# Kernel optimization log

Measured on AMD Instinct MI355X. Metric: run time of the kernel, lower is better.

The kernel has to match this reference:

```python
import jax, jax.numpy as jnp
import numpy as np

N_NODES = 65536
N_EDGES = 524288
N_LAYERS = 3
D = 128
ED = 32
BATCH = 64
NEG_SLOPE = 0.2


def setup_inputs() -> dict:
    key = jax.random.key(0)
    ks = jax.random.split(key, 10)
    w_scale = 1.0 / np.sqrt(D)
    return {
        "x": jax.random.normal(ks[0], (N_NODES, D), dtype=jnp.float32),
        "edge_index": jax.random.randint(ks[1], (2, N_EDGES), 0, N_NODES, dtype=jnp.int32),
        "edge_attr": jax.random.normal(ks[2], (N_EDGES, ED), dtype=jnp.float32),
        "Ws": jax.random.normal(ks[3], (N_LAYERS, D, D), dtype=jnp.float32) * w_scale,
        "att_src": jax.random.normal(ks[4], (N_LAYERS, D), dtype=jnp.float32) * w_scale,
        "att_dst": jax.random.normal(ks[5], (N_LAYERS, D), dtype=jnp.float32) * w_scale,
        "W_edge": jax.random.normal(ks[6], (N_LAYERS, ED, D), dtype=jnp.float32) * (1.0 / np.sqrt(ED)),
        "att_edge": jax.random.normal(ks[7], (N_LAYERS, D), dtype=jnp.float32) * w_scale,
        "bias": jnp.zeros((N_LAYERS, D), dtype=jnp.float32),
        "batch_size": BATCH,
    }


def _gat_layer(x, src, dst, ea, W, a_s, a_d, We, a_e, b, n):
    # PyG GATConv, heads=1, concat=True, flow source_to_target.
    h = x @ W                                      # [N, D]
    al = (h @ a_s)[src] + (h @ a_d)[dst] + (ea @ We) @ a_e   # [E]
    al = jax.nn.leaky_relu(al, NEG_SLOPE)
    # segment softmax over destination-node neighborhoods
    m = jax.ops.segment_max(al, dst, num_segments=n)
    ex = jnp.exp(al - m[dst])
    den = jax.ops.segment_sum(ex, dst, num_segments=n)
    w = ex / den[dst]                              # [E]
    out = jax.ops.segment_sum(w[:, None] * h[src], dst, num_segments=n)
    return out + b


def reference(x, edge_index, edge_attr, Ws, att_src, att_dst, W_edge, att_edge, bias, batch_size):
    n = x.shape[0]
    # add_self_loops with fill_value='mean': self-loop edge_attr is the mean of
    # incoming edge features per destination node (zero if no incoming edges).
    loop = jnp.arange(n, dtype=edge_index.dtype)
    src = jnp.concatenate([edge_index[0], loop])
    dst = jnp.concatenate([edge_index[1], loop])
    cnt = jax.ops.segment_sum(jnp.ones((edge_attr.shape[0],), edge_attr.dtype), edge_index[1], num_segments=n)
    fill = jax.ops.segment_sum(edge_attr, edge_index[1], num_segments=n) / jnp.maximum(cnt, 1.0)[:, None]
    ea = jnp.concatenate([edge_attr, fill], axis=0)

    h = x
    for l in range(Ws.shape[0]):
        h = jax.nn.gelu(
            _gat_layer(h, src, dst, ea, Ws[l], att_src[l], att_dst[l], W_edge[l], att_edge[l], bias[l], n),
            approximate=False,
        )
        # dropout p=0.2 is identity in eval mode
    return h.reshape(batch_size, n // batch_size, -1)
```

## Files before the change

### kernel.cpp

```cpp
#include <hip/hip_runtime.h>
#include <math.h>

#define NN 65536
#define NE 524288
#define D 128
#define ED 32
#define NEG_SLOPE 0.2f

typedef short bf16x8 __attribute__((ext_vector_type(8)));
typedef float f32x4 __attribute__((ext_vector_type(4)));
typedef unsigned short ushort_t;

__device__ __forceinline__ float leaky(float x) { return x > 0.f ? x : NEG_SLOPE * x; }
__device__ __forceinline__ float gelu_exact(float x) {
    return 0.5f * x * (1.f + erff(x * 0.70710678118654752440f));
}
__device__ __forceinline__ unsigned short bf16_rne(float x) {
    unsigned u = __float_as_uint(x);
    return (unsigned short)((u + 0x7FFFu + ((u >> 16) & 1u)) >> 16);
}
__device__ __forceinline__ void unpack8(int4 r, float* f) {
    unsigned u0 = (unsigned)r.x, u1 = (unsigned)r.y, u2 = (unsigned)r.z, u3 = (unsigned)r.w;
    f[0] = __uint_as_float(u0 << 16); f[1] = __uint_as_float(u0 & 0xFFFF0000u);
    f[2] = __uint_as_float(u1 << 16); f[3] = __uint_as_float(u1 & 0xFFFF0000u);
    f[4] = __uint_as_float(u2 << 16); f[5] = __uint_as_float(u2 & 0xFFFF0000u);
    f[6] = __uint_as_float(u3 << 16); f[7] = __uint_as_float(u3 & 0xFFFF0000u);
}


__global__ __launch_bounds__(256) void k_front(const float* __restrict__ ea,
        const int* __restrict__ dstArr, int* __restrict__ deg,
        const float* __restrict__ We, const float* __restrict__ ae,
        const float* __restrict__ Ws, short* __restrict__ Whp, short* __restrict__ Wlp,
        float* __restrict__ ale0, float* __restrict__ ale1, float* __restrict__ ale2) {
    if (blockIdx.x >= NE / 256) {
        int t = (blockIdx.x - NE / 256) * 256 + threadIdx.x;
        if (t >= 3 * 4 * 4 * 128) return;
        int n = t & 127;
        int q = (t >> 7) & 3;
        int ks = (t >> 9) & 3;
        int l = t >> 11;
        const float* w = Ws + (size_t)l * D * D;
        size_t obase = (size_t)l * D * D + ((size_t)((ks * 4 + q) * 128) + n) * 8;
        #pragma unroll
        for (int j = 0; j < 8; ++j) {
            float x = w[(size_t)(ks * 32 + q * 8 + j) * D + n];
            unsigned short hb = bf16_rne(x);
            float hf = __uint_as_float(((unsigned)hb) << 16);
            Whp[obase + j] = (short)hb;
            Wlp[obase + j] = (short)bf16_rne(x - hf);
        }
        return;
    }
    __shared__ __align__(16) float wv[3 * ED];
    int t = threadIdx.x;
    if (t < 3 * ED) {
        int l = t >> 5, k = t & 31;
        const float4* w = (const float4*)(We + (size_t)(l * ED + k) * D);
        const float4* a = (const float4*)(ae + (size_t)l * D);
        float s = 0.f;
        #pragma unroll
        for (int i = 0; i < D / 4; ++i) {
            float4 x = w[i], y = a[i];
            s += x.x * y.x + x.y * y.y + x.z * y.z + x.w * y.w;
        }
        wv[t] = s;
    }
    __syncthreads();
    int e = blockIdx.x * 256 + t;
    atomicAdd(&deg[dstArr[e]], 1);
    const float4* row = (const float4*)(ea + (size_t)e * ED);
    const float4* w0 = (const float4*)(wv);
    const float4* w1 = (const float4*)(wv + ED);
    const float4* w2 = (const float4*)(wv + 2 * ED);
    float s0 = 0.f, s1 = 0.f, s2 = 0.f;
    #pragma unroll
    for (int i = 0; i < ED / 4; ++i) {
        float4 v = row[i];
        float4 a = w0[i], b = w1[i], c = w2[i];
        s0 += v.x * a.x + v.y * a.y + v.z * a.z + v.w * a.w;
        s1 += v.x * b.x + v.y * b.y + v.z * b.z + v.w * b.w;
        s2 += v.x * c.x + v.y * c.y + v.z * c.z + v.w * c.w;
    }
    ale0[e] = s0;
    ale1[e] = s1;
    ale2[e] = s2;
}


__global__ void k_scan1(const int* __restrict__ deg, int* __restrict__ rp, int* __restrict__ bsum) {
    __shared__ int s[256];
    int t = threadIdx.x;
    int i = blockIdx.x * 256 + t;
    int v = deg[i];
    s[t] = v;
    __syncthreads();
    #pragma unroll
    for (int off = 1; off < 256; off <<= 1) {
        int x = (t >= off) ? s[t - off] : 0;
        __syncthreads();
        s[t] += x;
        __syncthreads();
    }
    rp[i] = s[t] - v;
    if (t == 255) bsum[blockIdx.x] = s[t];
}

__global__ void k_scanF(int* __restrict__ rp, const int* __restrict__ bsum, int* __restrict__ cursor) {
    __shared__ int s[256];
    int t = threadIdx.x;
    int bid = blockIdx.x;
    int v = bsum[t];
    s[t] = v;
    __syncthreads();
    #pragma unroll
    for (int off = 1; off < 256; off <<= 1) {
        int x = (t >= off) ? s[t - off] : 0;
        __syncthreads();
        s[t] += x;
        __syncthreads();
    }
    int add = (bid > 0) ? s[bid - 1] : 0;
    int i = bid * 256 + t;
    int r = rp[i] + add;
    rp[i] = r;
    cursor[i] = r;
    if (bid == 255 && t == 255) rp[NN] = NE;
}


__device__ __forceinline__ void gemm_body(int b, const float* __restrict__ A,
        const short* __restrict__ Whp, const short* __restrict__ Wlp,
        const float* __restrict__ a_s, const float* __restrict__ a_d,
        ushort_t* __restrict__ Hb, float* __restrict__ als, float* __restrict__ ald) {
    __shared__ int4 Bs[2048];
    int t = threadIdx.x;
    int wave = t >> 6, lane = t & 63;
    int l16 = lane & 15, q = lane >> 4;
    int rows_base = b * 64 + wave * 16;

    const int4* wh4 = (const int4*)Whp;
    const int4* wl4 = (const int4*)Wlp;
    const short* bsh = (const short*)Bs;
    const short* bsl = (const short*)(Bs + 1024);

    f32x4 acc[8] = {};
    #pragma unroll
    for (int h2 = 0; h2 < 2; ++h2) {
        if (h2) __syncthreads();
        #pragma unroll
        for (int i = 0; i < 4; ++i) {
            Bs[t + 256 * i] = wh4[h2 * 1024 + t + 256 * i];
            Bs[1024 + t + 256 * i] = wl4[h2 * 1024 + t + 256 * i];
        }
        __syncthreads();
        #pragma unroll
        for (int kk = 0; kk < 2; ++kk) {
            int ks = h2 * 2 + kk;
            const float* ap = A + (size_t)(rows_base + l16) * D + ks * 32 + q * 8;
            float4 v0 = *(const float4*)ap;
            float4 v1 = *(const float4*)(ap + 4);
            float f[8] = {v0.x, v0.y, v0.z, v0.w, v1.x, v1.y, v1.z, v1.w};
            bf16x8 ah, alo;
            #pragma unroll
            for (int j = 0; j < 8; ++j) {
                unsigned short hb = bf16_rne(f[j]);
                float hf = __uint_as_float(((unsigned)hb) << 16);
                ah[j]  = (short)hb;
                alo[j] = (short)bf16_rne(f[j] - hf);
            }
            #pragma unroll
            for (int nt = 0; nt < 8; ++nt) {
                int idx = (((kk * 4 + q) * 128) + nt * 16 + l16) * 8;
                bf16x8 bh = *(const bf16x8*)(bsh + idx);
                bf16x8 bl = *(const bf16x8*)(bsl + idx);
                acc[nt] = __builtin_amdgcn_mfma_f32_16x16x32_bf16(bh, ah, acc[nt], 0, 0, 0);
                acc[nt] = __builtin_amdgcn_mfma_f32_16x16x32_bf16(bl, ah, acc[nt], 0, 0, 0);
                acc[nt] = __builtin_amdgcn_mfma_f32_16x16x32_bf16(bh, alo, acc[nt], 0, 0, 0);
            }
        }
    }

    float ps = 0.f, pd = 0.f;
    #pragma unroll
    for (int nt = 0; nt < 8; ++nt) {
        float4 a4 = *(const float4*)(a_s + nt * 16 + q * 4);
        float4 d4 = *(const float4*)(a_d + nt * 16 + q * 4);
        ps += acc[nt][0] * a4.x + acc[nt][1] * a4.y + acc[nt][2] * a4.z + acc[nt][3] * a4.w;
        pd += acc[nt][0] * d4.x + acc[nt][1] * d4.y + acc[nt][2] * d4.z + acc[nt][3] * d4.w;
    }
    ps += __shfl_xor(ps, 16); pd += __shfl_xor(pd, 16);
    ps += __shfl_xor(ps, 32); pd += __shfl_xor(pd, 32);
    if (q == 0) {
        als[rows_base + l16] = ps;
        ald[rows_base + l16] = pd;
    }

    __syncthreads();
    char* tb = (char*)Bs + wave * 4096;
    {
        int row = l16;
        unsigned key = (unsigned)(row & 7) << 4;
        #pragma unroll
        for (int nt = 0; nt < 8; ++nt) {
            ushort4 pk;
            pk.x = bf16_rne(acc[nt][0]);
            pk.y = bf16_rne(acc[nt][1]);
            pk.z = bf16_rne(acc[nt][2]);
            pk.w = bf16_rne(acc[nt][3]);
            unsigned byteoff = (unsigned)row * 256u + (unsigned)(nt * 16 + q * 4) * 2u;
            *(ushort4*)(tb + (byteoff ^ key)) = pk;
        }
    }
    __syncthreads();
    #pragma unroll
    for (int i = 0; i < 4; ++i) {
        int m = lane + 64 * i;
        unsigned row = (unsigned)m >> 4;
        unsigned byteoff = (unsigned)m * 16u;
        unsigned addr = byteoff ^ ((row & 7u) << 4);
        int4 v = *(const int4*)(tb + addr);
        *(int4*)((char*)Hb + (size_t)rows_base * 256 + (size_t)m * 16) = v;
    }
}

__global__ __launch_bounds__(256) void k_scatgemm(
        const int* __restrict__ srcArr, const int* __restrict__ dstArr,
        int* __restrict__ cursor, const float* __restrict__ ale0,
        const float* __restrict__ ale1, const float* __restrict__ ale2,
        int4* __restrict__ edata,
        const float* __restrict__ A, const short* __restrict__ Whp,
        const short* __restrict__ Wlp, const float* __restrict__ a_s,
        const float* __restrict__ a_d, ushort_t* __restrict__ Hb,
        float* __restrict__ als, float* __restrict__ ald) {
    if (blockIdx.x < 256) {
        int base = blockIdx.x * 2048 + threadIdx.x;
        int e[8], d[8], p[8];
        #pragma unroll
        for (int i = 0; i < 8; ++i) e[i] = base + 256 * i;
        #pragma unroll
        for (int i = 0; i < 8; ++i) d[i] = dstArr[e[i]];
        #pragma unroll
        for (int i = 0; i < 8; ++i) p[i] = atomicAdd(&cursor[d[i]], 1);
        #pragma unroll
        for (int i = 0; i < 8; ++i) {
            edata[p[i]] = make_int4(srcArr[e[i]], __float_as_int(ale0[e[i]]),
                                    __float_as_int(ale1[e[i]]), __float_as_int(ale2[e[i]]));
        }
        return;
    }
    gemm_body(blockIdx.x - 256, A, Whp, Wlp, a_s, a_d, Hb, als, ald);
}

__global__ __launch_bounds__(256) void k_gemm(const float* __restrict__ A,
        const short* __restrict__ Whp, const short* __restrict__ Wlp,
        const float* __restrict__ a_s, const float* __restrict__ a_d,
        ushort_t* __restrict__ Hb, float* __restrict__ als, float* __restrict__ ald) {
    gemm_body(blockIdx.x, A, Whp, Wlp, a_s, a_d, Hb, als, ald);
}


__global__ __launch_bounds__(256) void k_aggr_fused(const ushort_t* __restrict__ hb,
        const float* __restrict__ als, const float* __restrict__ ald,
        const int4* __restrict__ edata, const int* __restrict__ rp,
        const float* __restrict__ bias, int lsel, float* __restrict__ out_f32) {
    int t = threadIdx.x;
    int lane = t & 63;
    int l16 = lane & 15;
    int qb = lane & 48;
    int n = blockIdx.x * 16 + (t >> 4);
    int s = rp[n], e = rp[n + 1];
    int deg = e - s;
    float aldd = ald[n];
    float alsn = als[n];
    float inv_deg = (deg > 0) ? 1.f / (float)deg : 0.f;

    int4 hvp = *(const int4*)(hb + (size_t)n * D + l16 * 8);
    float acc8[8];

    if (deg <= 16) {
        int sn0 = 0;
        float al0 = -1e30f, alev0 = 0.f;
        if (l16 < deg) {
            int4 ed = edata[s + l16];
            sn0 = ed.x;
            alev0 = __int_as_float((lsel == 0) ? ed.y : ((lsel == 1) ? ed.z : ed.w));
            al0 = leaky(als[sn0] + aldd + alev0);
        }
        float mm = al0, asum = alev0;
        #pragma unroll
        for (int off = 1; off < 16; off <<= 1) {
            mm = fmaxf(mm, __shfl_xor(mm, off));
            asum += __shfl_xor(asum, off);
        }
        float self_al = leaky(alsn + aldd + asum * inv_deg);
        mm = fmaxf(mm, self_al);
        float p0 = (l16 < deg) ? __expf(al0 - mm) : 0.f;
        float den = p0;
        #pragma unroll
        for (int off = 1; off < 16; off <<= 1) den += __shfl_xor(den, off);
        float es = __expf(self_al - mm);
        den += es;
        float inv = 1.f / den;
        float w0 = p0 * inv;
        float wself = es * inv;

        float fv[8];
        unpack8(hvp, fv);
        #pragma unroll
        for (int j = 0; j < 8; ++j) acc8[j] = wself * fv[j];

        int sA[8]; float wA[8]; int4 rb[8];
        #pragma unroll
        for (int i = 0; i < 8; ++i) { sA[i] = __shfl(sn0, qb + i); wA[i] = __shfl(w0, qb + i); }
        #pragma unroll
        for (int i = 0; i < 8; ++i) rb[i] = *(const int4*)(hb + (size_t)sA[i] * D + l16 * 8);

        int sB[8]; float wB[8]; int4 rb2[8];
        #pragma unroll
        for (int i = 0; i < 8; ++i) { sB[i] = __shfl(sn0, qb + 8 + i); wB[i] = __shfl(w0, qb + 8 + i); }
        bool more = (deg > 8);
        if (more) {
            #pragma unroll
            for (int i = 0; i < 8; ++i) rb2[i] = *(const int4*)(hb + (size_t)sB[i] * D + l16 * 8);
        }

        #pragma unroll
        for (int i = 0; i < 8; ++i) {
            float f[8];
            unpack8(rb[i], f);
            #pragma unroll
            for (int j = 0; j < 8; ++j) acc8[j] += wA[i] * f[j];
        }
        if (more) {
            #pragma unroll
            for (int i = 0; i < 8; ++i) {
                float f[8];
                unpack8(rb2[i], f);
                #pragma unroll
                for (int j = 0; j < 8; ++j) acc8[j] += wB[i] * f[j];
            }
        }
    } else {
        float mm = -1e30f, asum = 0.f;
        for (int base = s; base < e; base += 16) {
            int j = base + l16;
            if (j < e) {
                int4 ed = edata[j];
                float alev = __int_as_float((lsel == 0) ? ed.y : ((lsel == 1) ? ed.z : ed.w));
                asum += alev;
                mm = fmaxf(mm, leaky(als[ed.x] + aldd + alev));
            }
        }
        #pragma unroll
        for (int off = 1; off < 16; off <<= 1) {
            mm = fmaxf(mm, __shfl_xor(mm, off));
            asum += __shfl_xor(asum, off);
        }
        float self_al = leaky(alsn + aldd + asum * inv_deg);
        mm = fmaxf(mm, self_al);
        float den = 0.f;
        for (int base = s; base < e; base += 16) {
            int j = base + l16;
            if (j < e) {
                int4 ed = edata[j];
                float alev = __int_as_float((lsel == 0) ? ed.y : ((lsel == 1) ? ed.z : ed.w));
                den += __expf(leaky(als[ed.x] + aldd + alev) - mm);
            }
        }
        #pragma unroll
        for (int off = 1; off < 16; off <<= 1) den += __shfl_xor(den, off);
        float es = __expf(self_al - mm);
        den += es;
        float inv = 1.f / den;
        float wself = es * inv;
        float fv[8];
        unpack8(hvp, fv);
        #pragma unroll
        for (int j = 0; j < 8; ++j) acc8[j] = wself * fv[j];
        for (int base = s; base < e; base += 16) {
            int cnt = min(e - base, 16);
            int sn = 0;
            float w = 0.f;
            if (l16 < cnt) {
                int4 ed = edata[base + l16];
                sn = ed.x;
                float alev = __int_as_float((lsel == 0) ? ed.y : ((lsel == 1) ? ed.z : ed.w));
                w = __expf(leaky(als[sn] + aldd + alev) - mm) * inv;
            }
            for (int tt = 0; tt < cnt; ++tt) {
                int st = __shfl(sn, qb + tt);
                float wt = __shfl(w, qb + tt);
                int4 r = *(const int4*)(hb + (size_t)st * D + l16 * 8);
                float f[8];
                unpack8(r, f);
                #pragma unroll
                for (int j = 0; j < 8; ++j) acc8[j] += wt * f[j];
            }
        }
    }

    const float4* b4 = (const float4*)(bias + l16 * 8);
    float4 b0 = b4[0], b1 = b4[1];
    float bb[8] = {b0.x, b0.y, b0.z, b0.w, b1.x, b1.y, b1.z, b1.w};
    float o[8];
    #pragma unroll
    for (int j = 0; j < 8; ++j) o[j] = gelu_exact(acc8[j] + bb[j]);

    float4* o4 = (float4*)(out_f32 + (size_t)n * D + l16 * 8);
    o4[0] = make_float4(o[0], o[1], o[2], o[3]);
    o4[1] = make_float4(o[4], o[5], o[6], o[7]);
}


extern "C" void kernel_launch(void* const* d_in, const int* in_sizes, int n_in,
                              void* d_out, int out_size, void* d_ws, size_t ws_size,
                              hipStream_t stream) {
    (void)in_sizes; (void)n_in; (void)out_size; (void)ws_size;
    const float* x        = (const float*)d_in[0];
    const int*   eidx     = (const int*)d_in[1];
    const float* ea       = (const float*)d_in[2];
    const float* Ws       = (const float*)d_in[3];
    const float* att_src  = (const float*)d_in[4];
    const float* att_dst  = (const float*)d_in[5];
    const float* W_edge   = (const float*)d_in[6];
    const float* att_edge = (const float*)d_in[7];
    const float* bias     = (const float*)d_in[8];
    float* out = (float*)d_out;

    char* ws = (char*)d_ws;
    size_t off = 0;
    auto alloc = [&](size_t bytes) {
        void* p = ws + off;
        off += (bytes + 255) & ~(size_t)255;
        return p;
    };
    ushort_t* Hb   = (ushort_t*)alloc((size_t)NN * D * 2);
    float*    Hx   = (float*)alloc((size_t)NN * D * 4);
    float*    als  = (float*)alloc((size_t)NN * 4);
    float*    ald  = (float*)alloc((size_t)NN * 4);
    int4*     edata= (int4*)alloc((size_t)NE * 16);
    float*    ale0 = (float*)alloc((size_t)NE * 4);
    float*    ale1 = (float*)alloc((size_t)NE * 4);
    float*    ale2 = (float*)alloc((size_t)NE * 4);
    int*      deg  = (int*)alloc((size_t)NN * 4);
    int*      rp   = (int*)alloc((size_t)(NN + 4) * 4);
    int*      cursor = (int*)alloc((size_t)NN * 4);
    int*      bsum = (int*)alloc(256 * 4);
    short*    Whp  = (short*)alloc((size_t)3 * D * D * 2);
    short*    Wlp  = (short*)alloc((size_t)3 * D * D * 2);

    const int* e_src = eidx;
    const int* e_dst = eidx + NE;

    hipMemsetAsync(deg, 0, (size_t)NN * 4, stream);
    k_front<<<NE / 256 + 24, 256, 0, stream>>>(ea, e_dst, deg, W_edge, att_edge,
                                               Ws, Whp, Wlp, ale0, ale1, ale2);
    k_scan1<<<NN / 256, 256, 0, stream>>>(deg, rp, bsum);
    k_scanF<<<NN / 256, 256, 0, stream>>>(rp, bsum, cursor);

    k_scatgemm<<<256 + NN / 64, 256, 0, stream>>>(e_src, e_dst, cursor, ale0, ale1, ale2, edata,
                                                  x, Whp, Wlp, att_src, att_dst, Hb, als, ald);

    for (int l = 0; l < 3; ++l) {
        if (l > 0) {
            k_gemm<<<NN / 64, 256, 0, stream>>>(Hx, Whp + (size_t)l * D * D, Wlp + (size_t)l * D * D,
                                                att_src + (size_t)l * D, att_dst + (size_t)l * D,
                                                Hb, als, ald);
        }
        bool last = (l == 2);
        k_aggr_fused<<<NN / 16, 256, 0, stream>>>(Hb, als, ald, edata, rp, bias + (size_t)l * D, l,
                                                  last ? out : Hx);
    }
}
```

Before: 351.1 us.

## Fuse aggregation with next-layer GEMM and merge edge scatter into first GEMM

Layers 0 and 1 now aggregate 64 nodes per block into shared memory and feed that tile straight into the next layer's split-bf16 MFMA GEMM. This removes the fp32 Hx round-trip through global memory and two kernel launches. The CSR edge scatter moves from separate blocks into every GEMM-0 block, with each block handling 512 edges. H buffers are ping-ponged to avoid read/write hazards. The costs are 48KB of LDS per block, which lowers occupancy, and fewer blocks (64 nodes each) during the latency-bound gather phase.

```diff
diff --git a/kernel.cpp b/kernel.cpp
--- a/kernel.cpp
+++ b/kernel.cpp
@@ -129,15 +129,172 @@
 }
 
 
-__device__ __forceinline__ void gemm_body(int b, const float* __restrict__ A,
+__device__ __forceinline__ void aggr_node(int n, int l16, int qb,
+        const ushort_t* __restrict__ hb, const float* __restrict__ als,
+        const float* __restrict__ ald, const int4* __restrict__ edata,
+        const int* __restrict__ rp, const float* __restrict__ bias, int lsel,
+        float* o) {
+    int s = rp[n], e = rp[n + 1];
+    int deg = e - s;
+    float aldd = ald[n];
+    float alsn = als[n];
+    float inv_deg = (deg > 0) ? 1.f / (float)deg : 0.f;
+
+    int4 hvp = *(const int4*)(hb + (size_t)n * D + l16 * 8);
+    float acc8[8];
+
+    if (deg <= 16) {
+        int sn0 = 0;
+        float al0 = -1e30f, alev0 = 0.f;
+        if (l16 < deg) {
+            int4 ed = edata[s + l16];
+            sn0 = ed.x;
+            alev0 = __int_as_float((lsel == 0) ? ed.y : ((lsel == 1) ? ed.z : ed.w));
+            al0 = leaky(als[sn0] + aldd + alev0);
+        }
+        float mm = al0, asum = alev0;
+        #pragma unroll
+        for (int off = 1; off < 16; off <<= 1) {
+            mm = fmaxf(mm, __shfl_xor(mm, off));
+            asum += __shfl_xor(asum, off);
+        }
+        float self_al = leaky(alsn + aldd + asum * inv_deg);
+        mm = fmaxf(mm, self_al);
+        float p0 = (l16 < deg) ? __expf(al0 - mm) : 0.f;
+        float den = p0;
+        #pragma unroll
+        for (int off = 1; off < 16; off <<= 1) den += __shfl_xor(den, off);
+        float es = __expf(self_al - mm);
+        den += es;
+        float inv = 1.f / den;
+        float w0 = p0 * inv;
+        float wself = es * inv;
+
+        float fv[8];
+        unpack8(hvp, fv);
+        #pragma unroll
+        for (int j = 0; j < 8; ++j) acc8[j] = wself * fv[j];
+
+        int sA[8]; float wA[8]; int4 rb[8];
+        #pragma unroll
+        for (int i = 0; i < 8; ++i) { sA[i] = __shfl(sn0, qb + i); wA[i] = __shfl(w0, qb + i); }
+        #pragma unroll
+        for (int i = 0; i < 8; ++i) rb[i] = *(const int4*)(hb + (size_t)sA[i] * D + l16 * 8);
+
+        int sB[8]; float wB[8]; int4 rb2[8];
+        #pragma unroll
+        for (int i = 0; i < 8; ++i) { sB[i] = __shfl(sn0, qb + 8 + i); wB[i] = __shfl(w0, qb + 8 + i); }
+        bool more = (deg > 8);
+        if (more) {
+            #pragma unroll
+            for (int i = 0; i < 8; ++i) rb2[i] = *(const int4*)(hb + (size_t)sB[i] * D + l16 * 8);
+        }
+
+        #pragma unroll
+        for (int i = 0; i < 8; ++i) {
+            float f[8];
+            unpack8(rb[i], f);
+            #pragma unroll
+            for (int j = 0; j < 8; ++j) acc8[j] += wA[i] * f[j];
+        }
+        if (more) {
+            #pragma unroll
+            for (int i = 0; i < 8; ++i) {
+                float f[8];
+                unpack8(rb2[i], f);
+                #pragma unroll
+                for (int j = 0; j < 8; ++j) acc8[j] += wB[i] * f[j];
+            }
+        }
+    } else {
+        float mm = -1e30f, asum = 0.f;
+        for (int base = s; base < e; base += 16) {
+            int j = base + l16;
+            if (j < e) {
+                int4 ed = edata[j];
+                float alev = __int_as_float((lsel == 0) ? ed.y : ((lsel == 1) ? ed.z : ed.w));
+                asum += alev;
+                mm = fmaxf(mm, leaky(als[ed.x] + aldd + alev));
+            }
+        }
+        #pragma unroll
+        for (int off = 1; off < 16; off <<= 1) {
+            mm = fmaxf(mm, __shfl_xor(mm, off));
+            asum += __shfl_xor(asum, off);
+        }
+        float self_al = leaky(alsn + aldd + asum * inv_deg);
+        mm = fmaxf(mm, self_al);
+        float den = 0.f;
+        for (int base = s; base < e; base += 16) {
+            int j = base + l16;
+            if (j < e) {
+                int4 ed = edata[j];
+                float alev = __int_as_float((lsel == 0) ? ed.y : ((lsel == 1) ? ed.z : ed.w));
+                den += __expf(leaky(als[ed.x] + aldd + alev) - mm);
+            }
+        }
+        #pragma unroll
+        for (int off = 1; off < 16; off <<= 1) den += __shfl_xor(den, off);
+        float es = __expf(self_al - mm);
+        den += es;
+        float inv = 1.f / den;
+        float wself = es * inv;
+        float fv[8];
+        unpack8(hvp, fv);
+        #pragma unroll
+        for (int j = 0; j < 8; ++j) acc8[j] = wself * fv[j];
+        for (int base = s; base < e; base += 16) {
+            int cnt = min(e - base, 16);
+            int sn = 0;
+            float w = 0.f;
+            if (l16 < cnt) {
+                int4 ed = edata[base + l16];
+                sn = ed.x;
+                float alev = __int_as_float((lsel == 0) ? ed.y : ((lsel == 1) ? ed.z : ed.w));
+                w = __expf(leaky(als[sn] + aldd + alev) - mm) * inv;
+            }
+            for (int tt = 0; tt < cnt; ++tt) {
+                int st = __shfl(sn, qb + tt);
+                float wt = __shfl(w, qb + tt);
+                int4 r = *(const int4*)(hb + (size_t)st * D + l16 * 8);
+                float f[8];
+                unpack8(r, f);
+                #pragma unroll
+                for (int j = 0; j < 8; ++j) acc8[j] += wt * f[j];
+            }
+        }
+    }
+
+    const float4* b4 = (const float4*)(bias + l16 * 8);
+    float4 b0 = b4[0], b1 = b4[1];
+    float bb[8] = {b0.x, b0.y, b0.z, b0.w, b1.x, b1.y, b1.z, b1.w};
+    #pragma unroll
+    for (int j = 0; j < 8; ++j) o[j] = gelu_exact(acc8[j] + bb[j]);
+}
+
+
+__global__ __launch_bounds__(256) void k_gemm0scat(const float* __restrict__ A,
         const short* __restrict__ Whp, const short* __restrict__ Wlp,
         const float* __restrict__ a_s, const float* __restrict__ a_d,
-        ushort_t* __restrict__ Hb, float* __restrict__ als, float* __restrict__ ald) {
+        ushort_t* __restrict__ Hb, float* __restrict__ als, float* __restrict__ ald,
+        const int* __restrict__ srcArr, const int* __restrict__ dstArr,
+        int* __restrict__ cursor, const float* __restrict__ ale0,
+        const float* __restrict__ ale1, const float* __restrict__ ale2,
+        int4* __restrict__ edata) {
     __shared__ int4 Bs[2048];
     int t = threadIdx.x;
     int wave = t >> 6, lane = t & 63;
     int l16 = lane & 15, q = lane >> 4;
+    int b = blockIdx.x;
     int rows_base = b * 64 + wave * 16;
+
+    int e0 = b * 512 + t, e1 = e0 + 256;
+    int d0 = dstArr[e0], d1 = dstArr[e1];
+    int p0 = atomicAdd(&cursor[d0], 1);
+    int p1 = atomicAdd(&cursor[d1], 1);
+    int s0 = srcArr[e0], s1 = srcArr[e1];
+    float a00 = ale0[e0], a01 = ale1[e0], a02 = ale2[e0];
+    float a10 = ale0[e1], a11 = ale1[e1], a12 = ale2[e1];
 
     const int4* wh4 = (const int4*)Whp;
     const int4* wl4 = (const int4*)Wlp;
@@ -181,6 +338,9 @@
         }
     }
 
+    edata[p0] = make_int4(s0, __float_as_int(a00), __float_as_int(a01), __float_as_int(a02));
+    edata[p1] = make_int4(s1, __float_as_int(a10), __float_as_int(a11), __float_as_int(a12));
+
     float ps = 0.f, pd = 0.f;
     #pragma unroll
     for (int nt = 0; nt < 8; ++nt) {
@@ -224,43 +384,123 @@
     }
 }
 
-__global__ __launch_bounds__(256) void k_scatgemm(
-        const int* __restrict__ srcArr, const int* __restrict__ dstArr,
-        int* __restrict__ cursor, const float* __restrict__ ale0,
-        const float* __restrict__ ale1, const float* __restrict__ ale2,
-        int4* __restrict__ edata,
-        const float* __restrict__ A, const short* __restrict__ Whp,
-        const short* __restrict__ Wlp, const float* __restrict__ a_s,
-        const float* __restrict__ a_d, ushort_t* __restrict__ Hb,
-        float* __restrict__ als, float* __restrict__ ald) {
-    if (blockIdx.x < 256) {
-        int base = blockIdx.x * 2048 + threadIdx.x;
-        int e[8], d[8], p[8];
-        #pragma unroll
-        for (int i = 0; i < 8; ++i) e[i] = base + 256 * i;
-        #pragma unroll
-        for (int i = 0; i < 8; ++i) d[i] = dstArr[e[i]];
-        #pragma unroll
-        for (int i = 0; i < 8; ++i) p[i] = atomicAdd(&cursor[d[i]], 1);
-        #pragma unroll
-        for (int i = 0; i < 8; ++i) {
-            edata[p[i]] = make_int4(srcArr[e[i]], __float_as_int(ale0[e[i]]),
-                                    __float_as_int(ale1[e[i]]), __float_as_int(ale2[e[i]]));
-        }
-        return;
-    }
-    gemm_body(blockIdx.x - 256, A, Whp, Wlp, a_s, a_d, Hb, als, ald);
-}
-
-__global__ __launch_bounds__(256) void k_gemm(const float* __restrict__ A,
+
+__global__ __launch_bounds__(256) void k_aggrgemm(const ushort_t* __restrict__ hb,
+        const float* __restrict__ als_in, const float* __restrict__ ald_in,
+        const int4* __restrict__ edata, const int* __restrict__ rp,
+        const float* __restrict__ bias, int lsel,
         const short* __restrict__ Whp, const short* __restrict__ Wlp,
         const float* __restrict__ a_s, const float* __restrict__ a_d,
-        ushort_t* __restrict__ Hb, float* __restrict__ als, float* __restrict__ ald) {
-    gemm_body(blockIdx.x, A, Whp, Wlp, a_s, a_d, Hb, als, ald);
-}
-
-
-__global__ __launch_bounds__(256) void k_aggr_fused(const ushort_t* __restrict__ hb,
+        ushort_t* __restrict__ Hb_out, float* __restrict__ als_out,
+        float* __restrict__ ald_out) {
+    __shared__ __align__(16) char Abuf[32768];
+    __shared__ int4 Wst[1024];
+    int t = threadIdx.x;
+    int lane = t & 63;
+    int l16 = lane & 15;
+    int qb = lane & 48;
+    int q = lane >> 4;
+    int wave = t >> 6;
+    int b = blockIdx.x;
+
+    #pragma unroll
+    for (int j = 0; j < 4; ++j) {
+        int nl = (t >> 4) + 16 * j;
+        int n = b * 64 + nl;
+        float o[8];
+        aggr_node(n, l16, qb, hb, als_in, ald_in, edata, rp, bias, lsel, o);
+        unsigned key = (unsigned)(nl & 7) << 4;
+        unsigned bo = (unsigned)nl * 512u + (unsigned)l16 * 32u;
+        *(float4*)(Abuf + ((bo) ^ key)) = make_float4(o[0], o[1], o[2], o[3]);
+        *(float4*)(Abuf + ((bo + 16) ^ key)) = make_float4(o[4], o[5], o[6], o[7]);
+    }
+    __syncthreads();
+
+    int rows_base = b * 64 + wave * 16;
+    int rl = wave * 16 + l16;
+    unsigned akey = (unsigned)(rl & 7) << 4;
+    const int4* wh4 = (const int4*)Whp;
+    const int4* wl4 = (const int4*)Wlp;
+    const short* bsh = (const short*)Wst;
+    const short* bsl = (const short*)(Wst + 512);
+
+    f32x4 acc[8] = {};
+    #pragma unroll
+    for (int ks = 0; ks < 4; ++ks) {
+        if (ks) __syncthreads();
+        Wst[t]       = wh4[ks * 512 + t];
+        Wst[t + 256] = wh4[ks * 512 + 256 + t];
+        Wst[512 + t]       = wl4[ks * 512 + t];
+        Wst[512 + t + 256] = wl4[ks * 512 + 256 + t];
+        __syncthreads();
+        unsigned abo = (unsigned)rl * 512u + (unsigned)(ks * 128 + q * 32);
+        float4 v0 = *(const float4*)(Abuf + ((abo) ^ akey));
+        float4 v1 = *(const float4*)(Abuf + ((abo + 16) ^ akey));
+        float f[8] = {v0.x, v0.y, v0.z, v0.w, v1.x, v1.y, v1.z, v1.w};
+        bf16x8 ah, alo;
+        #pragma unroll
+        for (int j = 0; j < 8; ++j) {
+            unsigned short hb16 = bf16_rne(f[j]);
+            float hf = __uint_as_float(((unsigned)hb16) << 16);
+            ah[j]  = (short)hb16;
+            alo[j] = (short)bf16_rne(f[j] - hf);
+        }
+        #pragma unroll
+        for (int nt = 0; nt < 8; ++nt) {
+            int idx = (q * 128 + nt * 16 + l16) * 8;
+            bf16x8 bh = *(const bf16x8*)(bsh + idx);
+            bf16x8 bl = *(const bf16x8*)(bsl + idx);
+            acc[nt] = __builtin_amdgcn_mfma_f32_16x16x32_bf16(bh, ah, acc[nt], 0, 0, 0);
+            acc[nt] = __builtin_amdgcn_mfma_f32_16x16x32_bf16(bl, ah, acc[nt], 0, 0, 0);
+            acc[nt] = __builtin_amdgcn_mfma_f32_16x16x32_bf16(bh, alo, acc[nt], 0, 0, 0);
+        }
+    }
+
+    float ps = 0.f, pd = 0.f;
+    #pragma unroll
+    for (int nt = 0; nt < 8; ++nt) {
+        float4 a4 = *(const float4*)(a_s + nt * 16 + q * 4);
+        float4 d4 = *(const float4*)(a_d + nt * 16 + q * 4);
+        ps += acc[nt][0] * a4.x + acc[nt][1] * a4.y + acc[nt][2] * a4.z + acc[nt][3] * a4.w;
+        pd += acc[nt][0] * d4.x + acc[nt][1] * d4.y + acc[nt][2] * d4.z + acc[nt][3] * d4.w;
+    }
+    ps += __shfl_xor(ps, 16); pd += __shfl_xor(pd, 16);
+    ps += __shfl_xor(ps, 32); pd += __shfl_xor(pd, 32);
+    if (q == 0) {
+        als_out[rows_base + l16] = ps;
+        ald_out[rows_base + l16] = pd;
+    }
+
+    __syncthreads();
+    char* tb = Abuf + wave * 4096;
+    {
+        int row = l16;
+        unsigned key = (unsigned)(row & 7) << 4;
+        #pragma unroll
+        for (int nt = 0; nt < 8; ++nt) {
+            ushort4 pk;
+            pk.x = bf16_rne(acc[nt][0]);
+            pk.y = bf16_rne(acc[nt][1]);
+            pk.z = bf16_rne(acc[nt][2]);
+            pk.w = bf16_rne(acc[nt][3]);
+            unsigned byteoff = (unsigned)row * 256u + (unsigned)(nt * 16 + q * 4) * 2u;
+            *(ushort4*)(tb + (byteoff ^ key)) = pk;
+        }
+    }
+    __syncthreads();
+    #pragma unroll
+    for (int i = 0; i < 4; ++i) {
+        int m = lane + 64 * i;
+        unsigned row = (unsigned)m >> 4;
+        unsigned byteoff = (unsigned)m * 16u;
+        unsigned addr = byteoff ^ ((row & 7u) << 4);
+        int4 v = *(const int4*)(tb + addr);
+        *(int4*)((char*)Hb_out + (size_t)rows_base * 256 + (size_t)m * 16) = v;
+    }
+}
+
+
+__global__ __launch_bounds__(256) void k_aggr_final(const ushort_t* __restrict__ hb,
         const float* __restrict__ als, const float* __restrict__ ald,
         const int4* __restrict__ edata, const int* __restrict__ rp,
         const float* __restrict__ bias, int lsel, float* __restrict__ out_f32) {
@@ -269,144 +509,8 @@
     int l16 = lane & 15;
     int qb = lane & 48;
     int n = blockIdx.x * 16 + (t >> 4);
-    int s = rp[n], e = rp[n + 1];
-    int deg = e - s;
-    float aldd = ald[n];
-    float alsn = als[n];
-    float inv_deg = (deg > 0) ? 1.f / (float)deg : 0.f;
-
-    int4 hvp = *(const int4*)(hb + (size_t)n * D + l16 * 8);
-    float acc8[8];
-
-    if (deg <= 16) {
-        int sn0 = 0;
-        float al0 = -1e30f, alev0 = 0.f;
-        if (l16 < deg) {
-            int4 ed = edata[s + l16];
-            sn0 = ed.x;
-            alev0 = __int_as_float((lsel == 0) ? ed.y : ((lsel == 1) ? ed.z : ed.w));
-            al0 = leaky(als[sn0] + aldd + alev0);
-        }
-        float mm = al0, asum = alev0;
-        #pragma unroll
-        for (int off = 1; off < 16; off <<= 1) {
-            mm = fmaxf(mm, __shfl_xor(mm, off));
-            asum += __shfl_xor(asum, off);
-        }
-        float self_al = leaky(alsn + aldd + asum * inv_deg);
-        mm = fmaxf(mm, self_al);
-        float p0 = (l16 < deg) ? __expf(al0 - mm) : 0.f;
-        float den = p0;
-        #pragma unroll
-        for (int off = 1; off < 16; off <<= 1) den += __shfl_xor(den, off);
-        float es = __expf(self_al - mm);
-        den += es;
-        float inv = 1.f / den;
-        float w0 = p0 * inv;
-        float wself = es * inv;
-
-        float fv[8];
-        unpack8(hvp, fv);
-        #pragma unroll
-        for (int j = 0; j < 8; ++j) acc8[j] = wself * fv[j];
-
-        int sA[8]; float wA[8]; int4 rb[8];
-        #pragma unroll
-        for (int i = 0; i < 8; ++i) { sA[i] = __shfl(sn0, qb + i); wA[i] = __shfl(w0, qb + i); }
-        #pragma unroll
-        for (int i = 0; i < 8; ++i) rb[i] = *(const int4*)(hb + (size_t)sA[i] * D + l16 * 8);
-
-        int sB[8]; float wB[8]; int4 rb2[8];
-        #pragma unroll
-        for (int i = 0; i < 8; ++i) { sB[i] = __shfl(sn0, qb + 8 + i); wB[i] = __shfl(w0, qb + 8 + i); }
-        bool more = (deg > 8);
-        if (more) {
-            #pragma unroll
-            for (int i = 0; i < 8; ++i) rb2[i] = *(const int4*)(hb + (size_t)sB[i] * D + l16 * 8);
-        }
-
-        #pragma unroll
-        for (int i = 0; i < 8; ++i) {
-            float f[8];
-            unpack8(rb[i], f);
-            #pragma unroll
-            for (int j = 0; j < 8; ++j) acc8[j] += wA[i] * f[j];
-        }
-        if (more) {
-            #pragma unroll
-            for (int i = 0; i < 8; ++i) {
-                float f[8];
-                unpack8(rb2[i], f);
-                #pragma unroll
-                for (int j = 0; j < 8; ++j) acc8[j] += wB[i] * f[j];
-            }
-        }
-    } else {
-        float mm = -1e30f, asum = 0.f;
-        for (int base = s; base < e; base += 16) {
-            int j = base + l16;
-            if (j < e) {
-                int4 ed = edata[j];
-                float alev = __int_as_float((lsel == 0) ? ed.y : ((lsel == 1) ? ed.z : ed.w));
-                asum += alev;
-                mm = fmaxf(mm, leaky(als[ed.x] + aldd + alev));
-            }
-        }
-        #pragma unroll
-        for (int off = 1; off < 16; off <<= 1) {
-            mm = fmaxf(mm, __shfl_xor(mm, off));
-            asum += __shfl_xor(asum, off);
-        }
-        float self_al = leaky(alsn + aldd + asum * inv_deg);
-        mm = fmaxf(mm, self_al);
-        float den = 0.f;
-        for (int base = s; base < e; base += 16) {
-            int j = base + l16;
-            if (j < e) {
-                int4 ed = edata[j];
-                float alev = __int_as_float((lsel == 0) ? ed.y : ((lsel == 1) ? ed.z : ed.w));
-                den += __expf(leaky(als[ed.x] + aldd + alev) - mm);
-            }
-        }
-        #pragma unroll
-        for (int off = 1; off < 16; off <<= 1) den += __shfl_xor(den, off);
-        float es = __expf(self_al - mm);
-        den += es;
-        float inv = 1.f / den;
-        float wself = es * inv;
-        float fv[8];
-        unpack8(hvp, fv);
-        #pragma unroll
-        for (int j = 0; j < 8; ++j) acc8[j] = wself * fv[j];
-        for (int base = s; base < e; base += 16) {
-            int cnt = min(e - base, 16);
-            int sn = 0;
-            float w = 0.f;
-            if (l16 < cnt) {
-                int4 ed = edata[base + l16];
-                sn = ed.x;
-                float alev = __int_as_float((lsel == 0) ? ed.y : ((lsel == 1) ? ed.z : ed.w));
-                w = __expf(leaky(als[sn] + aldd + alev) - mm) * inv;
-            }
-            for (int tt = 0; tt < cnt; ++tt) {
-                int st = __shfl(sn, qb + tt);
-                float wt = __shfl(w, qb + tt);
-                int4 r = *(const int4*)(hb + (size_t)st * D + l16 * 8);
-                float f[8];
-                unpack8(r, f);
-                #pragma unroll
-                for (int j = 0; j < 8; ++j) acc8[j] += wt * f[j];
-            }
-        }
-    }
-
-    const float4* b4 = (const float4*)(bias + l16 * 8);
-    float4 b0 = b4[0], b1 = b4[1];
-    float bb[8] = {b0.x, b0.y, b0.z, b0.w, b1.x, b1.y, b1.z, b1.w};
     float o[8];
-    #pragma unroll
-    for (int j = 0; j < 8; ++j) o[j] = gelu_exact(acc8[j] + bb[j]);
-
+    aggr_node(n, l16, qb, hb, als, ald, edata, rp, bias, lsel, o);
     float4* o4 = (float4*)(out_f32 + (size_t)n * D + l16 * 8);
     o4[0] = make_float4(o[0], o[1], o[2], o[3]);
     o4[1] = make_float4(o[4], o[5], o[6], o[7]);
@@ -435,10 +539,12 @@
         off += (bytes + 255) & ~(size_t)255;
         return p;
     };
-    ushort_t* Hb   = (ushort_t*)alloc((size_t)NN * D * 2);
-    float*    Hx   = (float*)alloc((size_t)NN * D * 4);
-    float*    als  = (float*)alloc((size_t)NN * 4);
-    float*    ald  = (float*)alloc((size_t)NN * 4);
+    ushort_t* HbA  = (ushort_t*)alloc((size_t)NN * D * 2);
+    ushort_t* HbB  = (ushort_t*)alloc((size_t)NN * D * 2);
+    float*    alsA = (float*)alloc((size_t)NN * 4);
+    float*    aldA = (float*)alloc((size_t)NN * 4);
+    float*    alsB = (float*)alloc((size_t)NN * 4);
+    float*    aldB = (float*)alloc((size_t)NN * 4);
     int4*     edata= (int4*)alloc((size_t)NE * 16);
     float*    ale0 = (float*)alloc((size_t)NE * 4);
     float*    ale1 = (float*)alloc((size_t)NE * 4);
@@ -459,17 +565,17 @@
     k_scan1<<<NN / 256, 256, 0, stream>>>(deg, rp, bsum);
     k_scanF<<<NN / 256, 256, 0, stream>>>(rp, bsum, cursor);
 
-    k_scatgemm<<<256 + NN / 64, 256, 0, stream>>>(e_src, e_dst, cursor, ale0, ale1, ale2, edata,
-                                                  x, Whp, Wlp, att_src, att_dst, Hb, als, ald);
-
-    for (int l = 0; l < 3; ++l) {
-        if (l > 0) {
-            k_gemm<<<NN / 64, 256, 0, stream>>>(Hx, Whp + (size_t)l * D * D, Wlp + (size_t)l * D * D,
-                                                att_src + (size_t)l * D, att_dst + (size_t)l * D,
-                                                Hb, als, ald);
-        }
-        bool last = (l == 2);
-        k_aggr_fused<<<NN / 16, 256, 0, stream>>>(Hb, als, ald, edata, rp, bias + (size_t)l * D, l,
-                                                  last ? out : Hx);
-    }
-}
+    k_gemm0scat<<<NN / 64, 256, 0, stream>>>(x, Whp, Wlp, att_src, att_dst,
+                                             HbA, alsA, aldA,
+                                             e_src, e_dst, cursor, ale0, ale1, ale2, edata);
+
+    k_aggrgemm<<<NN / 64, 256, 0, stream>>>(HbA, alsA, aldA, edata, rp, bias, 0,
+                                            Whp + (size_t)1 * D * D, Wlp + (size_t)1 * D * D,
+                                            att_src + D, att_dst + D,
+                                            HbB, alsB, aldB);
+    k_aggrgemm<<<NN / 64, 256, 0, stream>>>(HbB, alsB, aldB, edata, rp, bias + D, 1,
+                                            Whp + (size_t)2 * D * D, Wlp + (size_t)2 * D * D,
+                                            att_src + 2 * D, att_dst + 2 * D,
+                                            HbA, alsA, aldA);
+    k_aggr_final<<<NN / 16, 256, 0, stream>>>(HbA, alsA, aldA, edata, rp, bias + 2 * D, 2, out);
+}
```

Measured after the change: 361.9 us. 1.03x slower.

## Replace atomic CSR scatter with deterministic two-pass radix bucketing by destination

Applied to the files above, without the earlier changes.

Replaces the global-atomic degree count, two scans and cursor-atomic scatter with a two-level radix sort on destination node: per-block shared-memory histograms on the high byte, a column scan, a coarse scatter into buckets, then a per-bucket fine sort on the low byte that also writes row pointers. Edge records (src plus three edge-attention scalars) are packed once in edge order by the front kernel. This removes contended global atomics and the random scattered writes to edata, at the cost of more kernel launches and an extra pass through intermediate buffers. The aggregation kernel also issues its neighbour feature row loads before the softmax reductions so memory latency overlaps the shuffle work.

```diff
diff --git a/kernel.cpp b/kernel.cpp
--- a/kernel.cpp
+++ b/kernel.cpp
@@ -29,10 +29,10 @@
 
 
 __global__ __launch_bounds__(256) void k_front(const float* __restrict__ ea,
-        const int* __restrict__ dstArr, int* __restrict__ deg,
+        const int* __restrict__ srcArr,
         const float* __restrict__ We, const float* __restrict__ ae,
         const float* __restrict__ Ws, short* __restrict__ Whp, short* __restrict__ Wlp,
-        float* __restrict__ ale0, float* __restrict__ ale1, float* __restrict__ ale2) {
+        int4* __restrict__ edata_eo) {
     if (blockIdx.x >= NE / 256) {
         int t = (blockIdx.x - NE / 256) * 256 + threadIdx.x;
         if (t >= 3 * 4 * 4 * 128) return;
@@ -68,7 +68,6 @@
     }
     __syncthreads();
     int e = blockIdx.x * 256 + t;
-    atomicAdd(&deg[dstArr[e]], 1);
     const float4* row = (const float4*)(ea + (size_t)e * ED);
     const float4* w0 = (const float4*)(wv);
     const float4* w1 = (const float4*)(wv + ED);
@@ -82,50 +81,7 @@
         s1 += v.x * b.x + v.y * b.y + v.z * b.z + v.w * b.w;
         s2 += v.x * c.x + v.y * c.y + v.z * c.z + v.w * c.w;
     }
-    ale0[e] = s0;
-    ale1[e] = s1;
-    ale2[e] = s2;
-}
-
-
-__global__ void k_scan1(const int* __restrict__ deg, int* __restrict__ rp, int* __restrict__ bsum) {
-    __shared__ int s[256];
-    int t = threadIdx.x;
-    int i = blockIdx.x * 256 + t;
-    int v = deg[i];
-    s[t] = v;
-    __syncthreads();
-    #pragma unroll
-    for (int off = 1; off < 256; off <<= 1) {
-        int x = (t >= off) ? s[t - off] : 0;
-        __syncthreads();
-        s[t] += x;
-        __syncthreads();
-    }
-    rp[i] = s[t] - v;
-    if (t == 255) bsum[blockIdx.x] = s[t];
-}
-
-__global__ void k_scanF(int* __restrict__ rp, const int* __restrict__ bsum, int* __restrict__ cursor) {
-    __shared__ int s[256];
-    int t = threadIdx.x;
-    int bid = blockIdx.x;
-    int v = bsum[t];
-    s[t] = v;
-    __syncthreads();
-    #pragma unroll
-    for (int off = 1; off < 256; off <<= 1) {
-        int x = (t >= off) ? s[t - off] : 0;
-        __syncthreads();
-        s[t] += x;
-        __syncthreads();
-    }
-    int add = (bid > 0) ? s[bid - 1] : 0;
-    int i = bid * 256 + t;
-    int r = rp[i] + add;
-    rp[i] = r;
-    cursor[i] = r;
-    if (bid == 255 && t == 255) rp[NN] = NE;
+    edata_eo[e] = make_int4(srcArr[e], __float_as_int(s0), __float_as_int(s1), __float_as_int(s2));
 }
 
 
@@ -224,33 +180,128 @@
     }
 }
 
-__global__ __launch_bounds__(256) void k_scatgemm(
-        const int* __restrict__ srcArr, const int* __restrict__ dstArr,
-        int* __restrict__ cursor, const float* __restrict__ ale0,
-        const float* __restrict__ ale1, const float* __restrict__ ale2,
-        int4* __restrict__ edata,
-        const float* __restrict__ A, const short* __restrict__ Whp,
+
+__global__ __launch_bounds__(256) void k_h1g0(const int* __restrict__ dstArr,
+        int* __restrict__ C,
+        const float* __restrict__ x, const short* __restrict__ Whp,
         const short* __restrict__ Wlp, const float* __restrict__ a_s,
         const float* __restrict__ a_d, ushort_t* __restrict__ Hb,
         float* __restrict__ als, float* __restrict__ ald) {
-    if (blockIdx.x < 256) {
-        int base = blockIdx.x * 2048 + threadIdx.x;
-        int e[8], d[8], p[8];
-        #pragma unroll
-        for (int i = 0; i < 8; ++i) e[i] = base + 256 * i;
-        #pragma unroll
-        for (int i = 0; i < 8; ++i) d[i] = dstArr[e[i]];
-        #pragma unroll
-        for (int i = 0; i < 8; ++i) p[i] = atomicAdd(&cursor[d[i]], 1);
-        #pragma unroll
-        for (int i = 0; i < 8; ++i) {
-            edata[p[i]] = make_int4(srcArr[e[i]], __float_as_int(ale0[e[i]]),
-                                    __float_as_int(ale1[e[i]]), __float_as_int(ale2[e[i]]));
-        }
+    int t = threadIdx.x;
+    if (blockIdx.x < 512) {
+        __shared__ int hist[256];
+        hist[t] = 0;
+        __syncthreads();
+        int base = blockIdx.x * 1024;
+        #pragma unroll
+        for (int i = 0; i < 4; ++i) {
+            int d = dstArr[base + i * 256 + t];
+            atomicAdd(&hist[d >> 8], 1);
+        }
+        __syncthreads();
+        C[blockIdx.x * 256 + t] = hist[t];
         return;
     }
-    gemm_body(blockIdx.x - 256, A, Whp, Wlp, a_s, a_d, Hb, als, ald);
-}
+    gemm_body(blockIdx.x - 512, x, Whp, Wlp, a_s, a_d, Hb, als, ald);
+}
+
+
+__global__ __launch_bounds__(256) void k_scanA(int* __restrict__ C, int* __restrict__ T) {
+    __shared__ int s[512];
+    int t = threadIdx.x, h = blockIdx.x;
+    int a0 = C[t * 256 + h];
+    int a1 = C[(t + 256) * 256 + h];
+    s[t] = a0; s[t + 256] = a1;
+    __syncthreads();
+    for (int off = 1; off < 512; off <<= 1) {
+        int v0 = (t >= off) ? s[t - off] : 0;
+        int v1 = (t + 256 >= off) ? s[t + 256 - off] : 0;
+        __syncthreads();
+        s[t] += v0; s[t + 256] += v1;
+        __syncthreads();
+    }
+    C[t * 256 + h] = s[t] - a0;
+    C[(t + 256) * 256 + h] = s[t + 256] - a1;
+    if (t == 255) T[h] = s[511];
+}
+
+
+__global__ __launch_bounds__(256) void k_scanB(const int* __restrict__ T, int* __restrict__ H,
+                                               int* __restrict__ rp) {
+    __shared__ int s[256];
+    int t = threadIdx.x;
+    int v = T[t];
+    s[t] = v;
+    __syncthreads();
+    for (int off = 1; off < 256; off <<= 1) {
+        int x = (t >= off) ? s[t - off] : 0;
+        __syncthreads();
+        s[t] += x;
+        __syncthreads();
+    }
+    H[t] = s[t] - v;
+    if (t == 255) { H[256] = s[255]; rp[NN] = s[255]; }
+}
+
+
+__global__ __launch_bounds__(256) void k_rank1(const int* __restrict__ dstArr,
+        const int4* __restrict__ edata_eo, const int* __restrict__ C,
+        const int* __restrict__ H, int4* __restrict__ eordR, int* __restrict__ eordD) {
+    __shared__ int base[256];
+    __shared__ int cnt[256];
+    int t = threadIdx.x, b = blockIdx.x;
+    base[t] = C[b * 256 + t] + H[t];
+    cnt[t] = 0;
+    __syncthreads();
+    #pragma unroll
+    for (int i = 0; i < 4; ++i) {
+        int e = b * 1024 + i * 256 + t;
+        int d = dstArr[e];
+        int4 rec = edata_eo[e];
+        int hi = d >> 8;
+        int r = atomicAdd(&cnt[hi], 1);
+        int p = base[hi] + r;
+        eordR[p] = rec;
+        eordD[p] = d;
+    }
+}
+
+
+__global__ __launch_bounds__(256) void k_rank2(const int* __restrict__ eordD,
+        const int4* __restrict__ eordR, const int* __restrict__ H,
+        int4* __restrict__ edata, int* __restrict__ rp) {
+    __shared__ int h2[256];
+    __shared__ int sc[256];
+    __shared__ int cnt[256];
+    int t = threadIdx.x, h = blockIdx.x;
+    int s0 = H[h], s1 = H[h + 1];
+    h2[t] = 0; cnt[t] = 0;
+    __syncthreads();
+    for (int i = s0 + t; i < s1; i += 256) atomicAdd(&h2[eordD[i] & 255], 1);
+    __syncthreads();
+    int v = h2[t];
+    sc[t] = v;
+    __syncthreads();
+    for (int off = 1; off < 256; off <<= 1) {
+        int x = (t >= off) ? sc[t - off] : 0;
+        __syncthreads();
+        sc[t] += x;
+        __syncthreads();
+    }
+    int baseLo = sc[t] - v;
+    rp[h * 256 + t] = s0 + baseLo;
+    __syncthreads();
+    sc[t] = baseLo;
+    __syncthreads();
+    for (int i = s0 + t; i < s1; i += 256) {
+        int d = eordD[i];
+        int4 rec = eordR[i];
+        int lo = d & 255;
+        int r = atomicAdd(&cnt[lo], 1);
+        edata[s0 + sc[lo] + r] = rec;
+    }
+}
+
 
 __global__ __launch_bounds__(256) void k_gemm(const float* __restrict__ A,
         const short* __restrict__ Whp, const short* __restrict__ Wlp,
@@ -260,7 +311,7 @@
 }
 
 
-__global__ __launch_bounds__(256) void k_aggr_fused(const ushort_t* __restrict__ hb,
+__global__ __launch_bounds__(256) void k_aggr(const ushort_t* __restrict__ hb,
         const float* __restrict__ als, const float* __restrict__ ald,
         const int4* __restrict__ edata, const int* __restrict__ rp,
         const float* __restrict__ bias, int lsel, float* __restrict__ out_f32) {
@@ -280,13 +331,28 @@
 
     if (deg <= 16) {
         int sn0 = 0;
-        float al0 = -1e30f, alev0 = 0.f;
+        float alev0 = 0.f, alsg = 0.f;
         if (l16 < deg) {
             int4 ed = edata[s + l16];
             sn0 = ed.x;
             alev0 = __int_as_float((lsel == 0) ? ed.y : ((lsel == 1) ? ed.z : ed.w));
-            al0 = leaky(als[sn0] + aldd + alev0);
-        }
+            alsg = als[sn0];
+        }
+
+        int sA[8], sB[8];
+        #pragma unroll
+        for (int i = 0; i < 8; ++i) { sA[i] = __shfl(sn0, qb + i); sB[i] = __shfl(sn0, qb + 8 + i); }
+        int4 rb[8];
+        #pragma unroll
+        for (int i = 0; i < 8; ++i) rb[i] = *(const int4*)(hb + (size_t)sA[i] * D + l16 * 8);
+        bool more = (deg > 8);
+        int4 rb2[8];
+        if (more) {
+            #pragma unroll
+            for (int i = 0; i < 8; ++i) rb2[i] = *(const int4*)(hb + (size_t)sB[i] * D + l16 * 8);
+        }
+
+        float al0 = (l16 < deg) ? leaky(alsg + aldd + alev0) : -1e30f;
         float mm = al0, asum = alev0;
         #pragma unroll
         for (int off = 1; off < 16; off <<= 1) {
@@ -310,20 +376,9 @@
         #pragma unroll
         for (int j = 0; j < 8; ++j) acc8[j] = wself * fv[j];
 
-        int sA[8]; float wA[8]; int4 rb[8];
-        #pragma unroll
-        for (int i = 0; i < 8; ++i) { sA[i] = __shfl(sn0, qb + i); wA[i] = __shfl(w0, qb + i); }
-        #pragma unroll
-        for (int i = 0; i < 8; ++i) rb[i] = *(const int4*)(hb + (size_t)sA[i] * D + l16 * 8);
-
-        int sB[8]; float wB[8]; int4 rb2[8];
-        #pragma unroll
-        for (int i = 0; i < 8; ++i) { sB[i] = __shfl(sn0, qb + 8 + i); wB[i] = __shfl(w0, qb + 8 + i); }
-        bool more = (deg > 8);
-        if (more) {
-            #pragma unroll
-            for (int i = 0; i < 8; ++i) rb2[i] = *(const int4*)(hb + (size_t)sB[i] * D + l16 * 8);
-        }
+        float wA[8], wB[8];
+        #pragma unroll
+        for (int i = 0; i < 8; ++i) { wA[i] = __shfl(w0, qb + i); wB[i] = __shfl(w0, qb + 8 + i); }
 
         #pragma unroll
         for (int i = 0; i < 8; ++i) {
@@ -439,37 +494,39 @@
     float*    Hx   = (float*)alloc((size_t)NN * D * 4);
     float*    als  = (float*)alloc((size_t)NN * 4);
     float*    ald  = (float*)alloc((size_t)NN * 4);
-    int4*     edata= (int4*)alloc((size_t)NE * 16);
-    float*    ale0 = (float*)alloc((size_t)NE * 4);
-    float*    ale1 = (float*)alloc((size_t)NE * 4);
-    float*    ale2 = (float*)alloc((size_t)NE * 4);
-    int*      deg  = (int*)alloc((size_t)NN * 4);
+    int4*     edata= (int4*)alloc((size_t)(NE + 16) * 16);
+    int4*     edata_eo = (int4*)alloc((size_t)NE * 16);
+    int4*     eordR = (int4*)alloc((size_t)NE * 16);
+    int*      eordD = (int*)alloc((size_t)NE * 4);
+    int*      C    = (int*)alloc((size_t)512 * 256 * 4);
+    int*      T    = (int*)alloc(256 * 4);
+    int*      H    = (int*)alloc(260 * 4);
     int*      rp   = (int*)alloc((size_t)(NN + 4) * 4);
-    int*      cursor = (int*)alloc((size_t)NN * 4);
-    int*      bsum = (int*)alloc(256 * 4);
     short*    Whp  = (short*)alloc((size_t)3 * D * D * 2);
     short*    Wlp  = (short*)alloc((size_t)3 * D * D * 2);
 
     const int* e_src = eidx;
     const int* e_dst = eidx + NE;
 
-    hipMemsetAsync(deg, 0, (size_t)NN * 4, stream);
-    k_front<<<NE / 256 + 24, 256, 0, stream>>>(ea, e_dst, deg, W_edge, att_edge,
-                                               Ws, Whp, Wlp, ale0, ale1, ale2);
-    k_scan1<<<NN / 256, 256, 0, stream>>>(deg, rp, bsum);
-    k_scanF<<<NN / 256, 256, 0, stream>>>(rp, bsum, cursor);
-
-    k_scatgemm<<<256 + NN / 64, 256, 0, stream>>>(e_src, e_dst, cursor, ale0, ale1, ale2, edata,
-                                                  x, Whp, Wlp, att_src, att_dst, Hb, als, ald);
+    k_front<<<NE / 256 + 24, 256, 0, stream>>>(ea, e_src, W_edge, att_edge,
+                                               Ws, Whp, Wlp, edata_eo);
+    k_h1g0<<<512 + NN / 64, 256, 0, stream>>>(e_dst, C, x, Whp, Wlp, att_src, att_dst,
+                                              Hb, als, ald);
+    k_scanA<<<256, 256, 0, stream>>>(C, T);
+    k_scanB<<<256 / 256, 256, 0, stream>>>(T, H, rp);
+    k_rank1<<<512, 256, 0, stream>>>(e_dst, edata_eo, C, H, eordR, eordD);
+    k_rank2<<<256, 256, 0, stream>>>(eordD, eordR, H, edata, rp);
 
     for (int l = 0; l < 3; ++l) {
-        if (l > 0) {
-            k_gemm<<<NN / 64, 256, 0, stream>>>(Hx, Whp + (size_t)l * D * D, Wlp + (size_t)l * D * D,
-                                                att_src + (size_t)l * D, att_dst + (size_t)l * D,
+        bool last = (l == 2);
+        k_aggr<<<NN / 16, 256, 0, stream>>>(Hb, als, ald, edata, rp, bias + (size_t)l * D, l,
+                                            last ? out : Hx);
+        if (!last) {
+            k_gemm<<<NN / 64, 256, 0, stream>>>(Hx, Whp + (size_t)(l + 1) * D * D,
+                                                Wlp + (size_t)(l + 1) * D * D,
+                                                att_src + (size_t)(l + 1) * D,
+                                                att_dst + (size_t)(l + 1) * D,
                                                 Hb, als, ald);
         }
-        bool last = (l == 2);
-        k_aggr_fused<<<NN / 16, 256, 0, stream>>>(Hb, als, ald, edata, rp, bias + (size_t)l * D, l,
-                                                  last ? out : Hx);
-    }
-}
+    }
+}
```

Measured after the change: 347.1 us. About the same (-1.1%).
